# Kernel optimization log

Measured on AMD Instinct MI355X. Metric: run time of the kernel, lower is better.

The kernel has to match this reference:

```python
import jax, jax.numpy as jnp
import numpy as np

N_NODES = 100000


def gcn_conv(x, W, b, src, dst, n_nodes):
    # PyG GCNConv: h = x @ W; add self-loops; norm = d^-1/2[src] * d^-1/2[dst];
    # aggregate sum of norm * h[src] at dst; then + bias.
    h = x @ W  # [N, F_out]
    loops = jnp.arange(n_nodes, dtype=src.dtype)
    s = jnp.concatenate([src, loops])  # [E+N]
    d = jnp.concatenate([dst, loops])
    deg = jax.ops.segment_sum(jnp.ones_like(d, dtype=h.dtype), d, num_segments=n_nodes)
    dinv = jax.lax.rsqrt(deg)  # deg >= 1 thanks to self-loops
    norm = dinv[s] * dinv[d]  # [E+N]
    msg = h[s] * norm[:, None]  # [E+N, F_out] -- large gather
    out = jax.ops.segment_sum(msg, d, num_segments=n_nodes)  # scatter-add
    return out + b


def setup_inputs() -> dict:
    key = jax.random.key(0)
    k = jax.random.split(key, 8)
    x = jax.random.normal(k[0], (N_NODES, 8), dtype=jnp.float32)
    edge_index = jax.random.randint(k[1], (2, 1600000), 0, N_NODES, dtype=jnp.int32)
    W1 = jax.random.normal(k[2], (8, 64), dtype=jnp.float32) * 0.3
    b1 = jnp.zeros((64,), dtype=jnp.float32)
    W2 = jax.random.normal(k[3], (64, 128), dtype=jnp.float32) * 0.1
    b2 = jnp.zeros((128,), dtype=jnp.float32)
    Wfc = jax.random.normal(k[4], (128, 1), dtype=jnp.float32) * 0.08
    bfc = jnp.zeros((1,), dtype=jnp.float32)
    return {"x": x, "edge_index": edge_index, "W1": W1, "b1": b1,
            "W2": W2, "b2": b2, "Wfc": Wfc, "bfc": bfc}


def reference(x, edge_index, W1, b1, W2, b2, Wfc, bfc):
    src, dst = edge_index[0], edge_index[1]
    n = x.shape[0]
    h = jax.nn.relu(gcn_conv(x, W1, b1, src, dst, n))   # dropout: eval mode (identity)
    h = jax.nn.relu(gcn_conv(h, W2, b2, src, dst, n))
    g = jnp.mean(h, axis=0)  # [128] graph readout
    return g @ Wfc + bfc     # [1]
```

## Files before the change

### kernel.cpp

```cpp
#include <hip/hip_runtime.h>


#define CHUNK 4096
#define NB_SHIFT 8
#define BCAP 5120
#define G2_GRID 1042

typedef float v2f __attribute__((ext_vector_type(2)));
typedef __bf16 bf16x8 __attribute__((ext_vector_type(8)));
typedef float f32x16 __attribute__((ext_vector_type(16)));

__device__ __forceinline__ unsigned short f2bf(float f) {
    unsigned u = __float_as_uint(f);
    return (unsigned short)((u + 0x7fffu + ((u >> 16) & 1u)) >> 16);
}
__device__ __forceinline__ unsigned pkbf(float a, float b) {
    return ((unsigned)f2bf(b) << 16) | f2bf(a);
}
__device__ __forceinline__ float bflo(unsigned u) { return __uint_as_float(u << 16); }
__device__ __forceinline__ float bfhi(unsigned u) { return __uint_as_float(u & 0xffff0000u); }
__device__ __forceinline__ bf16x8 asbf8(uint4 v) { return __builtin_bit_cast(bf16x8, v); }

__global__ __launch_bounds__(512) void scatterA(const int* __restrict__ ei, int E,
                                                int* __restrict__ cursor,
                                                unsigned int* __restrict__ bucketed) {
    __shared__ unsigned int pk[CHUNK];
    __shared__ unsigned short bk[CHUNK];
    __shared__ unsigned int spk[CHUNK];
    __shared__ unsigned short sbk[CHUNK];
    __shared__ int h[512], hsc[512], lcur[512], rbase[512];
    int tid = threadIdx.x;
    h[tid] = 0;
    lcur[tid] = 0;
    __syncthreads();
    int cbase = blockIdx.x * CHUNK;
    int cN = min(CHUNK, E - cbase);
    const int* src = ei;
    const int* dst = ei + E;
    for (int i = tid; i < cN; i += 512) {
        int s = src[cbase + i], d = dst[cbase + i];
        int b = d >> NB_SHIFT;
        pk[i] = (unsigned)s | ((unsigned)(d & 255) << 17);
        bk[i] = (unsigned short)b;
        atomicAdd(&h[b], 1);
    }
    __syncthreads();
    hsc[tid] = h[tid];
    __syncthreads();
    for (int off = 1; off < 512; off <<= 1) {
        int v0 = (tid >= off) ? hsc[tid - off] : 0;
        __syncthreads();
        hsc[tid] += v0;
        __syncthreads();
    }
    hsc[tid] -= h[tid];
    if (h[tid]) rbase[tid] = tid * BCAP + atomicAdd(&cursor[tid], h[tid]);
    __syncthreads();
    for (int i = tid; i < cN; i += 512) {
        int b = bk[i];
        int pos = hsc[b] + atomicAdd(&lcur[b], 1);
        spk[pos] = pk[i];
        sbk[pos] = (unsigned short)b;
    }
    __syncthreads();
    for (int p = tid; p < cN; p += 512) {
        int b = sbk[p];
        bucketed[rbase[b] + (p - hsc[b])] = spk[p];
    }
}

__global__ __launch_bounds__(512) void buildB(
    const unsigned int* __restrict__ bucketed, const int* __restrict__ cursor,
    int* __restrict__ row_start, int* __restrict__ cntg, float* __restrict__ dinv,
    int* __restrict__ csr_src, const float* __restrict__ x,
    unsigned int* __restrict__ xsb, int n) {
    __shared__ unsigned int spk[BCAP];
    __shared__ int scsr[BCAP];
    __shared__ int cnt[256], sc[256], cur[256];
    __shared__ float sdinv[256];
    int tid = threadIdx.x;
    int b = blockIdx.x;
    int s0 = b * BCAP;
    int m = cursor[b];
    if (tid < 256) cnt[tid] = 0;
    __syncthreads();
    for (int e = tid; e < m; e += 512) {
        unsigned v = bucketed[s0 + e];
        spk[e] = v;
        atomicAdd(&cnt[v >> 17], 1);
    }
    __syncthreads();
    if (tid < 256) sc[tid] = cnt[tid];
    __syncthreads();
    for (int off = 1; off < 256; off <<= 1) {
        int v0 = (tid < 256 && tid >= off) ? sc[tid - off] : 0;
        __syncthreads();
        if (tid < 256) sc[tid] += v0;
        __syncthreads();
    }
    int nb0 = b << NB_SHIFT;
    if (tid < 256) {
        int node = nb0 + tid;
        int ex = sc[tid] - cnt[tid];
        cur[tid] = ex;
        float dv = rsqrtf((float)cnt[tid] + 1.0f);
        sdinv[tid] = dv;
        if (node < n) {
            row_start[node] = s0 + ex;
            cntg[node] = cnt[tid];
            dinv[node] = dv;
        }
    }
    __syncthreads();
    for (int e = tid; e < m; e += 512) {
        unsigned v = spk[e];
        int r = atomicAdd(&cur[v >> 17], 1);
        scsr[r] = (int)(v & 0x1FFFFu);
    }
    __syncthreads();
    for (int e = tid; e < m; e += 512) csr_src[s0 + e] = scsr[e];
    int lim = min(n - nb0, 256) * 4;
    for (int i = tid; i < lim; i += 512) {
        float2 v = ((const float2*)x)[nb0 * 4 + i];
        float dvv = sdinv[i >> 2];
        xsb[nb0 * 4 + i] = pkbf(v.x * dvv, v.y * dvv);
    }
}

__global__ __launch_bounds__(256) void aggX_gemm1(
    const unsigned int* __restrict__ xsb, const float* __restrict__ dinv,
    const int* __restrict__ row_start, const int* __restrict__ cnt,
    const int* __restrict__ csr_src, const float* __restrict__ W1,
    const float* __restrict__ b1, unsigned int* __restrict__ h1q, int n) {
    __shared__ float w[512 + 64];
    __shared__ float axl[64 * 8];
    __shared__ float sdi[64];
    int tid = threadIdx.x;
    for (int i = tid; i < 512; i += 256) w[i] = W1[i];
    if (tid < 64) w[512 + tid] = b1[tid];
    int g = tid >> 2, l = tid & 3;
    int node = blockIdx.x * 64 + g;
    float a[8] = {};
    float di = 0.f;
    if (node < n) {
        di = dinv[node];
        const uint4* xs4 = (const uint4*)xsb;
        int e0 = row_start[node], e1 = e0 + cnt[node];
        int e = e0 + l;
        for (; e + 4 < e1; e += 8) {
            int sA = csr_src[e], sB = csr_src[e + 4];
            uint4 uA = xs4[sA], uB = xs4[sB];
            a[0] += bflo(uA.x) + bflo(uB.x);
            a[1] += bfhi(uA.x) + bfhi(uB.x);
            a[2] += bflo(uA.y) + bflo(uB.y);
            a[3] += bfhi(uA.y) + bfhi(uB.y);
            a[4] += bflo(uA.z) + bflo(uB.z);
            a[5] += bfhi(uA.z) + bfhi(uB.z);
            a[6] += bflo(uA.w) + bflo(uB.w);
            a[7] += bfhi(uA.w) + bfhi(uB.w);
        }
        for (; e < e1; e += 4) {
            uint4 u = xs4[csr_src[e]];
            a[0] += bflo(u.x); a[1] += bfhi(u.x);
            a[2] += bflo(u.y); a[3] += bfhi(u.y);
            a[4] += bflo(u.z); a[5] += bfhi(u.z);
            a[6] += bflo(u.w); a[7] += bfhi(u.w);
        }
        if (l == 0) {
            uint4 u = xs4[node];
            a[0] += bflo(u.x); a[1] += bfhi(u.x);
            a[2] += bflo(u.y); a[3] += bfhi(u.y);
            a[4] += bflo(u.z); a[5] += bfhi(u.z);
            a[6] += bflo(u.w); a[7] += bfhi(u.w);
        }
    }
#pragma unroll
    for (int k = 0; k < 8; k++) {
        a[k] += __shfl_xor(a[k], 1);
        a[k] += __shfl_xor(a[k], 2);
    }
    axl[g * 8 + 2 * l] = di * a[2 * l];
    axl[g * 8 + 2 * l + 1] = di * a[2 * l + 1];
    if (l == 0) sdi[g] = di;
    __syncthreads();
    int wv = tid >> 6, lane = tid & 63;
    int nb = blockIdx.x * 64;
    for (int it = 0; it < 16; it++) {
        int nl = wv * 16 + it;
        int nd = nb + nl;
        if (nd >= n) break;
        float h = w[512 + lane];
#pragma unroll
        for (int k = 0; k < 8; k++) h = fmaf(axl[nl * 8 + k], w[k * 64 + lane], h);
        float h1s = fmaxf(h, 0.f) * sdi[nl];
        unsigned word = ((unsigned)__builtin_amdgcn_cvt_pk_fp8_f32(h1s, h1s, 0, false)
                         & 0xFFu) << ((lane & 3) * 8);
        word |= __shfl_xor((int)word, 1);
        word |= __shfl_xor((int)word, 2);
        if ((lane & 3) == 0) h1q[nd * 16 + (lane >> 2)] = word;
    }
}

__global__ void agg64(const unsigned int* __restrict__ h1q, const float* __restrict__ dinv,
                      const int* __restrict__ row_start, const int* __restrict__ cnt,
                      const int* __restrict__ csr_src, uint2* __restrict__ ahb, int n) {
    int gid = blockIdx.x * blockDim.x + threadIdx.x;
    int node = gid >> 4;
    if (node >= n) return;
    int cq = threadIdx.x & 15;
    int es = cq >> 2, qp = cq & 3;
    const uint4* h4 = (const uint4*)h1q;
    float a[16] = {};
    int e0 = row_start[node], e1 = e0 + cnt[node];
    int e = e0 + es;
    for (; e + 4 < e1; e += 8) {
        int sA = csr_src[e], sB = csr_src[e + 4];
        uint4 uA = h4[sA * 4 + qp], uB = h4[sB * 4 + qp];
#pragma unroll
        for (int wdx = 0; wdx < 4; wdx++) {
            unsigned wa = (&uA.x)[wdx], wb = (&uB.x)[wdx];
            v2f la = __builtin_amdgcn_cvt_pk_f32_fp8((int)wa, false);
            v2f ha = __builtin_amdgcn_cvt_pk_f32_fp8((int)wa, true);
            v2f lb = __builtin_amdgcn_cvt_pk_f32_fp8((int)wb, false);
            v2f hb = __builtin_amdgcn_cvt_pk_f32_fp8((int)wb, true);
            a[wdx * 4 + 0] += la[0] + lb[0];
            a[wdx * 4 + 1] += la[1] + lb[1];
            a[wdx * 4 + 2] += ha[0] + hb[0];
            a[wdx * 4 + 3] += ha[1] + hb[1];
        }
    }
    for (; e < e1; e += 4) {
        uint4 u = h4[csr_src[e] * 4 + qp];
#pragma unroll
        for (int wdx = 0; wdx < 4; wdx++) {
            unsigned wu = (&u.x)[wdx];
            v2f lo = __builtin_amdgcn_cvt_pk_f32_fp8((int)wu, false);
            v2f hi = __builtin_amdgcn_cvt_pk_f32_fp8((int)wu, true);
            a[wdx * 4 + 0] += lo[0];
            a[wdx * 4 + 1] += lo[1];
            a[wdx * 4 + 2] += hi[0];
            a[wdx * 4 + 3] += hi[1];
        }
    }
    if (es == 0) {
        uint4 u = h4[node * 4 + qp];
#pragma unroll
        for (int wdx = 0; wdx < 4; wdx++) {
            unsigned wu = (&u.x)[wdx];
            v2f lo = __builtin_amdgcn_cvt_pk_f32_fp8((int)wu, false);
            v2f hi = __builtin_amdgcn_cvt_pk_f32_fp8((int)wu, true);
            a[wdx * 4 + 0] += lo[0];
            a[wdx * 4 + 1] += lo[1];
            a[wdx * 4 + 2] += hi[0];
            a[wdx * 4 + 3] += hi[1];
        }
    }
#pragma unroll
    for (int k = 0; k < 16; k++) {
        a[k] += __shfl_xor(a[k], 4);
        a[k] += __shfl_xor(a[k], 8);
    }
    if (es == 0) {
        float di = dinv[node];
        uint4 r0, r1;
        r0.x = pkbf(di * a[0], di * a[1]);
        r0.y = pkbf(di * a[2], di * a[3]);
        r0.z = pkbf(di * a[4], di * a[5]);
        r0.w = pkbf(di * a[6], di * a[7]);
        r1.x = pkbf(di * a[8], di * a[9]);
        r1.y = pkbf(di * a[10], di * a[11]);
        r1.z = pkbf(di * a[12], di * a[13]);
        r1.w = pkbf(di * a[14], di * a[15]);
        uint4* out4 = (uint4*)ahb;
        out4[node * 8 + qp * 2] = r0;
        out4[node * 8 + qp * 2 + 1] = r1;
    }
}

__global__ __launch_bounds__(256) void gemm2_fused(
    const uint2* __restrict__ ahb, const float* __restrict__ W2,
    const float* __restrict__ b2, const float* __restrict__ Wfc,
    float* __restrict__ partial, int n) {
    __shared__ __align__(16) uint4 wb4[4 * 4 * 64];
    __shared__ __align__(16) uint4 atp4[32 * 8];
    __shared__ float wsum[4];
    int tid = threadIdx.x;
    unsigned* wbd = (unsigned*)wb4;
    for (int i = tid; i < 4096; i += 256) {
        int j = i & 127;
        int r = i >> 7;
        int t = r >> 3, l5s = (r >> 2) & 1, d = r & 3;
        int k0 = 16 * t + 8 * l5s + 2 * d;
        unsigned val = pkbf(W2[k0 * 128 + j], W2[(k0 + 1) * 128 + j]);
        int w = j >> 5, lan = l5s * 32 + (j & 31);
        wbd[(((w * 4 + t) * 64) + lan) * 4 + d] = val;
    }
    __syncthreads();
    int lane = tid & 63;
    int w = tid >> 6;
    int col = lane & 31;
    int l5 = lane >> 5;
    uint4 bf0 = wb4[(w * 4 + 0) * 64 + lane];
    uint4 bf1 = wb4[(w * 4 + 1) * 64 + lane];
    uint4 bf2 = wb4[(w * 4 + 2) * 64 + lane];
    uint4 bf3 = wb4[(w * 4 + 3) * 64 + lane];
    float bj = b2[w * 32 + col];
    const uint4* ahb4 = (const uint4*)ahb;
    float colsum = 0.f;
    int ntiles = (n + 31) >> 5;
    for (int tt = blockIdx.x; tt < ntiles; tt += gridDim.x) {
        int base = tt * 32;
        __syncthreads();
        {
            int nl = tid >> 3, s = tid & 7;
            uint4 v = make_uint4(0u, 0u, 0u, 0u);
            if (base + nl < n) v = ahb4[(base + nl) * 8 + s];
            atp4[nl * 8 + (s ^ (nl & 7))] = v;
        }
        __syncthreads();
        f32x16 acc = {};
        {
            uint4 a0 = atp4[col * 8 + ((2 * 0 + l5) ^ (col & 7))];
            acc = __builtin_amdgcn_mfma_f32_32x32x16_bf16(asbf8(a0), asbf8(bf0), acc, 0, 0, 0);
            uint4 a1 = atp4[col * 8 + ((2 * 1 + l5) ^ (col & 7))];
            acc = __builtin_amdgcn_mfma_f32_32x32x16_bf16(asbf8(a1), asbf8(bf1), acc, 0, 0, 0);
            uint4 a2 = atp4[col * 8 + ((2 * 2 + l5) ^ (col & 7))];
            acc = __builtin_amdgcn_mfma_f32_32x32x16_bf16(asbf8(a2), asbf8(bf2), acc, 0, 0, 0);
            uint4 a3 = atp4[col * 8 + ((2 * 3 + l5) ^ (col & 7))];
            acc = __builtin_amdgcn_mfma_f32_32x32x16_bf16(asbf8(a3), asbf8(bf3), acc, 0, 0, 0);
        }
        int nvalid = n - base;
        if (nvalid >= 32) {
#pragma unroll
            for (int reg = 0; reg < 16; reg++) colsum += fmaxf(acc[reg] + bj, 0.f);
        } else {
#pragma unroll
            for (int reg = 0; reg < 16; reg++) {
                int rrow = (reg & 3) + 8 * (reg >> 2) + 4 * l5;
                if (rrow < nvalid) colsum += fmaxf(acc[reg] + bj, 0.f);
            }
        }
    }
    colsum += __shfl_xor(colsum, 32);
    float v = (l5 == 0) ? colsum * Wfc[w * 32 + col] : 0.f;
#pragma unroll
    for (int off = 1; off < 64; off <<= 1) v += __shfl_xor(v, off);
    if (lane == 0) wsum[w] = v;
    __syncthreads();
    if (tid == 0) partial[blockIdx.x] = wsum[0] + wsum[1] + wsum[2] + wsum[3];
}

__global__ __launch_bounds__(256) void finish_kernel(
    const float* __restrict__ partial, const float* __restrict__ bfc,
    float* __restrict__ out, float invN, int G) {
    __shared__ float sh[4];
    int tid = threadIdx.x;
    float s = 0.f;
    for (int b = tid; b < G; b += 256) s += partial[b];
#pragma unroll
    for (int off = 32; off > 0; off >>= 1) s += __shfl_down(s, off);
    if ((tid & 63) == 0) sh[tid >> 6] = s;
    __syncthreads();
    if (tid == 0) out[0] = (sh[0] + sh[1] + sh[2] + sh[3]) * invN + bfc[0];
}

extern "C" void kernel_launch(void* const* d_in, const int* in_sizes, int n_in,
                              void* d_out, int out_size, void* d_ws, size_t ws_size,
                              hipStream_t stream) {
    const float* x   = (const float*)d_in[0];
    const int* ei    = (const int*)d_in[1];
    const float* W1  = (const float*)d_in[2];
    const float* b1  = (const float*)d_in[3];
    const float* W2  = (const float*)d_in[4];
    const float* b2  = (const float*)d_in[5];
    const float* Wfc = (const float*)d_in[6];
    const float* bfc = (const float*)d_in[7];
    float* out = (float*)d_out;

    const int n = in_sizes[0] / 8;
    const int E = in_sizes[1] / 2;

    const int nA = (E + CHUNK - 1) / CHUNK;
    const int B = (n + 255) >> NB_SHIFT;

    char* ws = (char*)d_ws;
    size_t off = 0;
    auto alloc = [&](size_t bytes) -> char* {
        char* p = ws + off;
        off = (off + bytes + 255) & ~(size_t)255;
        return p;
    };
    int*            cursor    = (int*)alloc(512 * 4);
    unsigned int*   bucketed  = (unsigned int*)alloc((size_t)B * BCAP * 4);
    int*            row_start = (int*)alloc((size_t)n * 4);
    int*            cnt       = (int*)alloc((size_t)n * 4);
    float*          dinv      = (float*)alloc((size_t)n * 4);
    int*            csr_src   = (int*)alloc((size_t)B * BCAP * 4);
    unsigned int*   xsb       = (unsigned int*)alloc((size_t)n * 16);
    unsigned int*   h1q       = (unsigned int*)alloc((size_t)n * 64);
    uint2*          ahb       = (uint2*)alloc((size_t)n * 128);
    float*          partial   = (float*)alloc((size_t)G2_GRID * 4);
    (void)ws_size;

    hipMemsetAsync(cursor, 0, 512 * 4, stream);
    scatterA<<<nA, 512, 0, stream>>>(ei, E, cursor, bucketed);
    buildB<<<B, 512, 0, stream>>>(bucketed, cursor, row_start, cnt, dinv, csr_src,
                                  x, xsb, n);
    aggX_gemm1<<<(n + 63) / 64, 256, 0, stream>>>(xsb, dinv, row_start, cnt, csr_src,
                                                  W1, b1, h1q, n);
    agg64<<<(n * 16 + 255) / 256, 256, 0, stream>>>(h1q, dinv, row_start, cnt, csr_src,
                                                    ahb, n);
    gemm2_fused<<<G2_GRID, 256, 0, stream>>>(ahb, W2, b2, Wfc, partial, n);
    finish_kernel<<<1, 256, 0, stream>>>(partial, bfc, out, 1.0f / (float)n, G2_GRID);
}
```

Baseline: 156.3 us.

## Replace global-atomic bucket scatter with per-chunk sorted segments and offset table

scatterA now writes each chunk's locally bucket-sorted edges contiguously and records per-chunk bucket offsets, instead of claiming global slots per bucket with atomics and scattering. buildB scans the offset table across the chunks to gather its bucket's segments from every chunk, and the cursor memset goes away. This removes global atomics, the scattered writes and one launch, but buildB now does a 512-wide scan and a serial per-thread copy loop whose short, strided segments may coalesce poorly.

```diff
diff --git a/kernel.cpp b/kernel.cpp
--- a/kernel.cpp
+++ b/kernel.cpp
@@ -22,13 +22,12 @@
 __device__ __forceinline__ bf16x8 asbf8(uint4 v) { return __builtin_bit_cast(bf16x8, v); }
 
 __global__ __launch_bounds__(512) void scatterA(const int* __restrict__ ei, int E,
-                                                int* __restrict__ cursor,
+                                                int* __restrict__ offs,
                                                 unsigned int* __restrict__ bucketed) {
     __shared__ unsigned int pk[CHUNK];
     __shared__ unsigned short bk[CHUNK];
     __shared__ unsigned int spk[CHUNK];
-    __shared__ unsigned short sbk[CHUNK];
-    __shared__ int h[512], hsc[512], lcur[512], rbase[512];
+    __shared__ int h[512], hsc[512], lcur[512];
     int tid = threadIdx.x;
     h[tid] = 0;
     lcur[tid] = 0;
@@ -54,41 +53,52 @@
         __syncthreads();
     }
     hsc[tid] -= h[tid];
-    if (h[tid]) rbase[tid] = tid * BCAP + atomicAdd(&cursor[tid], h[tid]);
+    offs[blockIdx.x * 513 + tid] = hsc[tid];
+    if (tid == 0) offs[blockIdx.x * 513 + 512] = cN;
     __syncthreads();
     for (int i = tid; i < cN; i += 512) {
         int b = bk[i];
         int pos = hsc[b] + atomicAdd(&lcur[b], 1);
         spk[pos] = pk[i];
-        sbk[pos] = (unsigned short)b;
-    }
-    __syncthreads();
-    for (int p = tid; p < cN; p += 512) {
-        int b = sbk[p];
-        bucketed[rbase[b] + (p - hsc[b])] = spk[p];
-    }
+    }
+    __syncthreads();
+    for (int p = tid; p < cN; p += 512) bucketed[cbase + p] = spk[p];
 }
 
 __global__ __launch_bounds__(512) void buildB(
-    const unsigned int* __restrict__ bucketed, const int* __restrict__ cursor,
-    int* __restrict__ row_start, int* __restrict__ cntg, float* __restrict__ dinv,
-    int* __restrict__ csr_src, const float* __restrict__ x,
-    unsigned int* __restrict__ xsb, int n) {
+    const unsigned int* __restrict__ bucketed, const int* __restrict__ offs,
+    int nA, int* __restrict__ row_start, int* __restrict__ cntg,
+    float* __restrict__ dinv, int* __restrict__ csr_src,
+    const float* __restrict__ x, unsigned int* __restrict__ xsb, int n) {
     __shared__ unsigned int spk[BCAP];
     __shared__ int scsr[BCAP];
+    __shared__ int fsc[512];
     __shared__ int cnt[256], sc[256], cur[256];
     __shared__ float sdinv[256];
     int tid = threadIdx.x;
     int b = blockIdx.x;
-    int s0 = b * BCAP;
-    int m = cursor[b];
     if (tid < 256) cnt[tid] = 0;
-    __syncthreads();
-    for (int e = tid; e < m; e += 512) {
-        unsigned v = bucketed[s0 + e];
-        spk[e] = v;
-        atomicAdd(&cnt[v >> 17], 1);
-    }
+    int o0 = 0, len = 0;
+    if (tid < nA) {
+        o0 = offs[tid * 513 + b];
+        len = offs[tid * 513 + b + 1] - o0;
+    }
+    fsc[tid] = len;
+    __syncthreads();
+    for (int off = 1; off < 512; off <<= 1) {
+        int v0 = (tid >= off) ? fsc[tid - off] : 0;
+        __syncthreads();
+        fsc[tid] += v0;
+        __syncthreads();
+    }
+    int m = fsc[511];
+    {
+        int lb = fsc[tid] - len;
+        int gb = tid * CHUNK + o0;
+        for (int k = 0; k < len; k++) spk[lb + k] = bucketed[gb + k];
+    }
+    __syncthreads();
+    for (int e = tid; e < m; e += 512) atomicAdd(&cnt[spk[e] >> 17], 1);
     __syncthreads();
     if (tid < 256) sc[tid] = cnt[tid];
     __syncthreads();
@@ -99,6 +109,7 @@
         __syncthreads();
     }
     int nb0 = b << NB_SHIFT;
+    int s0 = b * BCAP;
     if (tid < 256) {
         int node = nb0 + tid;
         int ex = sc[tid] - cnt[tid];
@@ -390,8 +401,8 @@
         off = (off + bytes + 255) & ~(size_t)255;
         return p;
     };
-    int*            cursor    = (int*)alloc(512 * 4);
-    unsigned int*   bucketed  = (unsigned int*)alloc((size_t)B * BCAP * 4);
+    int*            offs      = (int*)alloc((size_t)nA * 513 * 4);
+    unsigned int*   bucketed  = (unsigned int*)alloc((size_t)nA * CHUNK * 4);
     int*            row_start = (int*)alloc((size_t)n * 4);
     int*            cnt       = (int*)alloc((size_t)n * 4);
     float*          dinv      = (float*)alloc((size_t)n * 4);
@@ -402,9 +413,8 @@
     float*          partial   = (float*)alloc((size_t)G2_GRID * 4);
     (void)ws_size;
 
-    hipMemsetAsync(cursor, 0, 512 * 4, stream);
-    scatterA<<<nA, 512, 0, stream>>>(ei, E, cursor, bucketed);
-    buildB<<<B, 512, 0, stream>>>(bucketed, cursor, row_start, cnt, dinv, csr_src,
+    scatterA<<<nA, 512, 0, stream>>>(ei, E, offs, bucketed);
+    buildB<<<B, 512, 0, stream>>>(bucketed, offs, nA, row_start, cnt, dinv, csr_src,
                                   x, xsb, n);
     aggX_gemm1<<<(n + 63) / 64, 256, 0, stream>>>(xsb, dinv, row_start, cnt, csr_src,
                                                   W1, b1, h1q, n);
```

Measured after the change: 155.4 us (median of 2 runs). No clear change (-0.6%).
